# Optimization experiments

Hardware: AMD Instinct MI355X
Metric: run time of the kernel (lower is better)

The kernel has to match this reference:

```python
import jax, jax.numpy as jnp
import numpy as np

BN_EPS = 1e-5


def setup_inputs() -> dict:
    key = jax.random.key(0)
    ks = jax.random.split(key, 6)
    N, E, D_IN, D_OUT = 100000, 625000, 128, 128
    x = jax.random.normal(ks[0], (N, D_IN), dtype=jnp.float32)
    edge_index = jax.random.randint(ks[1], (2, E), 0, N, dtype=jnp.int64)
    # Glorot-style init for GCNConv weight, uniform for linear (values only matter for correctness testing)
    W = jax.random.normal(ks[2], (D_IN, D_OUT), dtype=jnp.float32) * (1.0 / np.sqrt(D_IN))
    b = jnp.zeros((D_OUT,), dtype=jnp.float32)
    res_W = jax.random.normal(ks[3], (D_IN, D_OUT), dtype=jnp.float32) * (1.0 / np.sqrt(D_IN))
    res_b = jnp.zeros((D_OUT,), dtype=jnp.float32)
    bn_gamma = jnp.ones((D_OUT,), dtype=jnp.float32)
    bn_beta = jnp.zeros((D_OUT,), dtype=jnp.float32)
    return {"x": x, "edge_index": edge_index, "W": W, "b": b,
            "res_W": res_W, "res_b": res_b, "bn_gamma": bn_gamma, "bn_beta": bn_beta}


def _gcn_forward(x, edge_index, W, b, res_W, res_b, bn_gamma, bn_beta):
    N = x.shape[0]
    # ---- GCNConv: add self-loops, symmetric degree normalization (PyG defaults) ----
    loops = jnp.arange(N, dtype=edge_index.dtype)
    src = jnp.concatenate([edge_index[0], loops])  # row (source)
    dst = jnp.concatenate([edge_index[1], loops])  # col (target)
    ones = jnp.ones(src.shape[0], dtype=x.dtype)
    deg = jax.ops.segment_sum(ones, dst, num_segments=N)  # in-degree incl. self-loop
    deg_inv_sqrt = jnp.where(deg > 0, jax.lax.rsqrt(deg), 0.0)
    norm = deg_inv_sqrt[src] * deg_inv_sqrt[dst]  # [E+N]
    # transform first (dense GEMM), then gather/scale/scatter-add
    h = x @ W  # [N, D_OUT]
    msg = h[src] * norm[:, None]  # gather + scale
    agg = jax.ops.segment_sum(msg, dst, num_segments=N) + b  # scatter-add + bias
    # ---- residual: relu(linear(x)) ----
    res = jax.nn.relu(x @ res_W + res_b)
    y = agg + res
    # ---- dropout(p=0.0) is identity; BatchNorm1d (training mode, batch stats) ----
    mean = jnp.mean(y, axis=0)
    var = jnp.mean(jnp.square(y - mean), axis=0)  # biased variance, as in torch BN normalization
    y = (y - mean) * jax.lax.rsqrt(var + BN_EPS) * bn_gamma + bn_beta
    return y


def reference(x, edge_index, W, b, res_W, res_b, bn_gamma, bn_beta):
    return _gcn_forward(x, edge_index, W, b, res_W, res_b, bn_gamma, bn_beta)
```

## Files before the change

kernel.cpp:

```cpp
#include <hip/hip_runtime.h>
#include <math.h>

#define D 128
#define DW 64

typedef __attribute__((ext_vector_type(8))) short bf16x8;
typedef __attribute__((ext_vector_type(4))) float f32x4;
union U4 { uint4 u; bf16x8 f; };

__device__ __forceinline__ float blo(unsigned p){ return __uint_as_float(p << 16); }
__device__ __forceinline__ float bhi(unsigned p){ return __uint_as_float(p & 0xffff0000u); }
__device__ __forceinline__ unsigned bpack(float a, float b){
  unsigned x = __float_as_uint(a), y = __float_as_uint(b);
  x += 0x7fffu + ((x >> 16) & 1u);
  y += 0x7fffu + ((y >> 16) & 1u);
  return (x >> 16) | (y & 0xffff0000u);
}


__global__ void k_deg(const int* __restrict__ ei, int* __restrict__ cnt, int E){
  int e = blockIdx.x*256 + threadIdx.x;
  if (e < E) atomicAdd(cnt + ei[E + e], 1);
}

__global__ void k_scan1(const int* __restrict__ cnt, int* __restrict__ off,
                        int* __restrict__ bsum, int N){
  __shared__ int sm[256];
  int i = blockIdx.x*256 + threadIdx.x;
  int v = (i < N) ? cnt[i] : 0;
  int acc = v;
  sm[threadIdx.x] = acc;
  __syncthreads();
  for (int s = 1; s < 256; s <<= 1){
    int t = (threadIdx.x >= s) ? sm[threadIdx.x - s] : 0;
    __syncthreads();
    acc += t;
    sm[threadIdx.x] = acc;
    __syncthreads();
  }
  if (i < N) off[i] = acc - v;
  if (threadIdx.x == 255) bsum[blockIdx.x] = acc;
}

__global__ void k_scan2(int* __restrict__ bsum, int nb){
  __shared__ int sm[512];
  int v = (threadIdx.x < nb) ? bsum[threadIdx.x] : 0;
  int acc = v;
  sm[threadIdx.x] = acc;
  __syncthreads();
  for (int s = 1; s < 512; s <<= 1){
    int t = (threadIdx.x >= s) ? sm[threadIdx.x - s] : 0;
    __syncthreads();
    acc += t;
    sm[threadIdx.x] = acc;
    __syncthreads();
  }
  if (threadIdx.x < nb) bsum[threadIdx.x] = acc - v;
}

__global__ void k_scan3(int* __restrict__ off, const int* __restrict__ bsum,
                        int* __restrict__ cursor, int N){
  int i = blockIdx.x*256 + threadIdx.x;
  if (i < N){
    int o = off[i] + bsum[blockIdx.x];
    off[i] = o;
    cursor[i] = o;
  }
}

__global__ void k_prep(const float* __restrict__ x, const int* __restrict__ cnt,
                       unsigned* __restrict__ out_u, int N){
  int idx = blockIdx.x*256 + threadIdx.x;
  if (idx >= N*DW) return;
  int row = idx >> 6, col = idx & 63;
  float dis = rsqrtf((float)(cnt[row] + 1));
  float2 xv = reinterpret_cast<const float2*>(x)[idx];
  out_u[(size_t)row*128 + 64 + col] = bpack(xv.x * dis, xv.y * dis);
}

__global__ void k_wprep(const float* __restrict__ W, const float* __restrict__ RW,
                        unsigned* __restrict__ dst){
  int idx = blockIdx.x*256 + threadIdx.x;
  int m = idx >> 13;
  int w = idx & 8191;
  int c = w >> 6, kd = w & 63;
  const float* src = m ? RW : W;
  float a = src[(2*kd)*128 + c];
  float b = src[(2*kd+1)*128 + c];
  dst[(m<<13) + c*64 + (kd ^ ((c & 7) << 2))] = bpack(a, b);
}

__global__ void k_fill(const int* __restrict__ ei, int* __restrict__ cursor,
                       int* __restrict__ elist, int E){
  int e = blockIdx.x*256 + threadIdx.x;
  if (e < E){
    int d = ei[E + e];
    int pos = atomicAdd(cursor + d, 1);
    elist[pos] = ei[e];
  }
}

__global__ __launch_bounds__(256) void k_agg(unsigned* __restrict__ out_u,
    const int* __restrict__ elist, const int* __restrict__ off,
    const int* __restrict__ cnt, int N){
  const int lane = threadIdx.x & 63;
  int wid = blockIdx.x*4 + (threadIdx.x >> 6);
  const int nw = gridDim.x*4;
  for (int i = wid; i < N; i += nw){
    int node = __builtin_amdgcn_readfirstlane(i);
    int o = off[node];
    int c = cnt[node];
    float a0 = 0.f, a1 = 0.f;
    for (int j0 = 0; j0 < c; j0 += 64){
      int m = c - j0; if (m > 64) m = 64;
      int sid = (j0 + lane < c) ? elist[o + j0 + lane] : 0;
      for (int jj = 0; jj < m; ++jj){
        int s = __shfl(sid, jj);
        unsigned p = out_u[(size_t)s*128 + 64 + lane];
        a0 += blo(p); a1 += bhi(p);
      }
    }
    unsigned ps = out_u[(size_t)node*128 + 64 + lane];
    a0 += blo(ps); a1 += bhi(ps);
    float dis = rsqrtf((float)(c + 1));
    out_u[(size_t)node*128 + lane] = bpack(a0*dis, a1*dis);
  }
}

__global__ __launch_bounds__(512) void k_gemm(
    const unsigned* __restrict__ wsW,
    const float* __restrict__ bias, const float* __restrict__ rbias,
    const int* __restrict__ cnt,
    float* __restrict__ out, float* __restrict__ colsum, int N)
{
  __shared__ unsigned lds[16384];
  unsigned* out_u = reinterpret_cast<unsigned*>(out);
  for (int i = threadIdx.x; i < 16384; i += 512) lds[i] = wsW[i];
  __syncthreads();

  const int lane = threadIdx.x & 63;
  const int wave = threadIdx.x >> 6;
  const int lo = lane & 15, hi = lane >> 4;
  const int rowbase = (blockIdx.x * 8 + wave) * 16;

  float bcol[8], rbcol[8];
  #pragma unroll
  for (int ct = 0; ct < 8; ++ct){
    bcol[ct]  = bias[ct*16 + lo];
    rbcol[ct] = rbias[ct*16 + lo];
  }

  int arow = rowbase + lo; if (arow >= N) arow = N - 1;
  U4 aggF[4], xbF[4];
  #pragma unroll
  for (int kk = 0; kk < 4; ++kk){
    aggF[kk].u = *(const uint4*)&out_u[(size_t)arow*128 + kk*16 + hi*4];
    xbF[kk].u  = *(const uint4*)&out_u[(size_t)arow*128 + 64 + kk*16 + hi*4];
  }

  f32x4 accA[8], accR[8];
  #pragma unroll
  for (int ct = 0; ct < 8; ++ct){
    accA[ct] = (f32x4){0.f,0.f,0.f,0.f};
    accR[ct] = (f32x4){0.f,0.f,0.f,0.f};
  }

  #pragma unroll
  for (int ct = 0; ct < 8; ++ct){
    const int c = ct*16 + lo;
    #pragma unroll
    for (int kk = 0; kk < 4; ++kk){
      int kd = (kk*16 + hi*4) ^ ((c & 7) << 2);
      U4 wf, rf;
      wf.u = *(const uint4*)&lds[c*64 + kd];
      rf.u = *(const uint4*)&lds[8192 + c*64 + kd];
      accA[ct] = __builtin_amdgcn_mfma_f32_16x16x32_bf16(aggF[kk].f, wf.f, accA[ct], 0,0,0);
      accR[ct] = __builtin_amdgcn_mfma_f32_16x16x32_bf16(xbF[kk].f, rf.f, accR[ct], 0,0,0);
    }
  }

  float s_[4];
  #pragma unroll
  for (int j = 0; j < 4; ++j){
    int r = rowbase + hi*4 + j;
    int rc = r < N ? r : N - 1;
    s_[j] = sqrtf((float)(cnt[rc] + 1));
  }
  float cs[8], cq[8];
  #pragma unroll
  for (int ct = 0; ct < 8; ++ct){ cs[ct] = 0.f; cq[ct] = 0.f; }

  #pragma unroll
  for (int ct = 0; ct < 8; ++ct){
    const int col = ct*16 + lo;
    #pragma unroll
    for (int j = 0; j < 4; ++j){
      int r = rowbase + hi*4 + j;
      if (r < N){
        float y = accA[ct][j] + bcol[ct] + fmaxf(accR[ct][j]*s_[j] + rbcol[ct], 0.f);
        out[(size_t)r*128 + col] = y;
        cs[ct] += y; cq[ct] += y*y;
      }
    }
  }

  #pragma unroll
  for (int ct = 0; ct < 8; ++ct){
    cs[ct] += __shfl_xor(cs[ct], 16); cs[ct] += __shfl_xor(cs[ct], 32);
    cq[ct] += __shfl_xor(cq[ct], 16); cq[ct] += __shfl_xor(cq[ct], 32);
  }
  __syncthreads();
  float* red = reinterpret_cast<float*>(lds);
  if (lane < 16){
    #pragma unroll
    for (int ct = 0; ct < 8; ++ct){
      int col = ct*16 + lane;
      red[wave*256 + 2*col]     = cs[ct];
      red[wave*256 + 2*col + 1] = cq[ct];
    }
  }
  __syncthreads();
  if (threadIdx.x < 256){
    float t = 0.f;
    #pragma unroll
    for (int w = 0; w < 8; ++w) t += red[w*256 + threadIdx.x];
    atomicAdd(colsum + threadIdx.x, t);
  }
}

__global__ void k_bnfinal(const float* __restrict__ colsum, const float* __restrict__ gamma,
                          const float* __restrict__ beta, float* __restrict__ sc, float fN){
  int c = threadIdx.x;
  float mean = colsum[2*c] / fN;
  float var  = colsum[2*c + 1] / fN - mean*mean;
  var = fmaxf(var, 0.f);
  float inv = rsqrtf(var + 1e-5f);
  float s = gamma[c] * inv;
  sc[c] = s;
  sc[128 + c] = beta[c] - mean * s;
}

__global__ void k_norm(float4* __restrict__ out4, const float4* __restrict__ sc4, int n4){
  int idx = blockIdx.x*256 + threadIdx.x;
  int stride = gridDim.x*256;
  for (int i = idx; i < n4; i += stride){
    int cb = i & 31;
    float4 v = out4[i];
    float4 s = sc4[cb];
    float4 t = sc4[32 + cb];
    v.x = v.x*s.x + t.x; v.y = v.y*s.y + t.y;
    v.z = v.z*s.z + t.z; v.w = v.w*s.w + t.w;
    out4[i] = v;
  }
}

extern "C" void kernel_launch(void* const* d_in, const int* in_sizes, int n_in,
                              void* d_out, int out_size, void* d_ws, size_t ws_size,
                              hipStream_t stream){
  const float* x     = (const float*)d_in[0];
  const int*   ei    = (const int*)d_in[1];
  const float* W     = (const float*)d_in[2];
  const float* b     = (const float*)d_in[3];
  const float* RW    = (const float*)d_in[4];
  const float* rb    = (const float*)d_in[5];
  const float* gamma = (const float*)d_in[6];
  const float* beta  = (const float*)d_in[7];
  float* out = (float*)d_out;
  unsigned* out_u = (unsigned*)d_out;
  const int N = in_sizes[0] / D;
  const int E = in_sizes[1] / 2;

  char* ws = (char*)d_ws;
  size_t o = 0;
  auto alloc = [&](size_t bytes)->void*{
    void* p = ws + o;
    o += (bytes + 255) & ~size_t(255);
    return p;
  };
  int*      cnt    = (int*)alloc((size_t)N*4);
  int*      off    = (int*)alloc((size_t)N*4);
  int*      cursor = (int*)alloc((size_t)N*4);
  int*      bsum   = (int*)alloc(512*4);
  float*    colsum = (float*)alloc(256*4);
  float*    scale  = (float*)alloc(256*4);
  unsigned* wsW    = (unsigned*)alloc(16384*4);
  int*      elist  = (int*)alloc((size_t)E*4);

  hipMemsetAsync(cnt, 0, (size_t)N*4, stream);
  hipMemsetAsync(colsum, 0, 256*4, stream);

  int egrid = (E + 255)/256;
  int nb = (N + 255)/256;
  k_deg  <<<egrid, 256, 0, stream>>>(ei, cnt, E);
  k_scan1<<<nb,    256, 0, stream>>>(cnt, off, bsum, N);
  k_scan2<<<1,     512, 0, stream>>>(bsum, nb);
  k_scan3<<<nb,    256, 0, stream>>>(off, bsum, cursor, N);
  k_prep <<<(N*DW + 255)/256, 256, 0, stream>>>(x, cnt, out_u, N);
  k_wprep<<<64,    256, 0, stream>>>(W, RW, wsW);
  k_fill <<<egrid, 256, 0, stream>>>(ei, cursor, elist, E);
  k_agg  <<<4096,  256, 0, stream>>>(out_u, elist, off, cnt, N);
  k_gemm <<<(N + 127)/128, 512, 0, stream>>>(wsW, b, rb, cnt, out, colsum, N);
  k_bnfinal<<<1, 128, 0, stream>>>(colsum, gamma, beta, scale, (float)N);
  k_norm <<<2048, 256, 0, stream>>>((float4*)out, (const float4*)scale, N*32);
}
```

Measured before the change: 301.6 us.

## Unroll neighbor gathers, widen prep stores, fuse BN finalize into normalize

The aggregation loop now issues four independent neighbor-row loads per iteration instead of one, and hoists the self-row load, so more memory requests are in flight per wave. The prep kernel handles float4 inputs per thread and writes uint2 stores, halving its thread count. The separate BN-finalize launch is removed; every normalize block recomputes the per-column scale and shift into shared memory. The trade-offs are redundant scale computation in each of 2048 blocks and extra clamped or masked loads at tail iterations.

```diff
diff --git a/kernel.cpp b/kernel.cpp
--- a/kernel.cpp
+++ b/kernel.cpp
@@ -71,11 +71,12 @@
 __global__ void k_prep(const float* __restrict__ x, const int* __restrict__ cnt,
                        unsigned* __restrict__ out_u, int N){
   int idx = blockIdx.x*256 + threadIdx.x;
-  if (idx >= N*DW) return;
-  int row = idx >> 6, col = idx & 63;
+  if (idx >= N*32) return;
+  int row = idx >> 5, q = idx & 31;
   float dis = rsqrtf((float)(cnt[row] + 1));
-  float2 xv = reinterpret_cast<const float2*>(x)[idx];
-  out_u[(size_t)row*128 + 64 + col] = bpack(xv.x * dis, xv.y * dis);
+  float4 xv = reinterpret_cast<const float4*>(x)[idx];
+  uint2 r; r.x = bpack(xv.x*dis, xv.y*dis); r.y = bpack(xv.z*dis, xv.w*dis);
+  reinterpret_cast<uint2*>(out_u)[(size_t)row*64 + 32 + q] = r;
 }
 
 __global__ void k_wprep(const float* __restrict__ W, const float* __restrict__ RW,
@@ -110,17 +111,28 @@
     int node = __builtin_amdgcn_readfirstlane(i);
     int o = off[node];
     int c = cnt[node];
+    unsigned ps = out_u[(size_t)node*128 + 64 + lane];
     float a0 = 0.f, a1 = 0.f;
     for (int j0 = 0; j0 < c; j0 += 64){
       int m = c - j0; if (m > 64) m = 64;
-      int sid = (j0 + lane < c) ? elist[o + j0 + lane] : 0;
-      for (int jj = 0; jj < m; ++jj){
-        int s = __shfl(sid, jj);
-        unsigned p = out_u[(size_t)s*128 + 64 + lane];
-        a0 += blo(p); a1 += bhi(p);
+      int li = lane < m ? lane : m-1;
+      int sid = elist[o + j0 + li];
+      for (int jj = 0; jj < m; jj += 4){
+        int s0 = __shfl(sid, jj);
+        int s1 = __shfl(sid, jj+1 < m ? jj+1 : m-1);
+        int s2 = __shfl(sid, jj+2 < m ? jj+2 : m-1);
+        int s3 = __shfl(sid, jj+3 < m ? jj+3 : m-1);
+        unsigned p0 = out_u[(size_t)s0*128 + 64 + lane];
+        unsigned p1 = out_u[(size_t)s1*128 + 64 + lane];
+        unsigned p2 = out_u[(size_t)s2*128 + 64 + lane];
+        unsigned p3 = out_u[(size_t)s3*128 + 64 + lane];
+        if (jj+1 >= m) p1 = 0;
+        if (jj+2 >= m) p2 = 0;
+        if (jj+3 >= m) p3 = 0;
+        a0 += blo(p0) + blo(p1) + blo(p2) + blo(p3);
+        a1 += bhi(p0) + bhi(p1) + bhi(p2) + bhi(p3);
       }
     }
-    unsigned ps = out_u[(size_t)node*128 + 64 + lane];
     a0 += blo(ps); a1 += bhi(ps);
     float dis = rsqrtf((float)(c + 1));
     out_u[(size_t)node*128 + lane] = bpack(a0*dis, a1*dis);
@@ -228,26 +240,27 @@
   }
 }
 
-__global__ void k_bnfinal(const float* __restrict__ colsum, const float* __restrict__ gamma,
-                          const float* __restrict__ beta, float* __restrict__ sc, float fN){
-  int c = threadIdx.x;
-  float mean = colsum[2*c] / fN;
-  float var  = colsum[2*c + 1] / fN - mean*mean;
-  var = fmaxf(var, 0.f);
-  float inv = rsqrtf(var + 1e-5f);
-  float s = gamma[c] * inv;
-  sc[c] = s;
-  sc[128 + c] = beta[c] - mean * s;
-}
-
-__global__ void k_norm(float4* __restrict__ out4, const float4* __restrict__ sc4, int n4){
+__global__ void k_norm(float4* __restrict__ out4, const float* __restrict__ colsum,
+                       const float* __restrict__ gamma, const float* __restrict__ beta,
+                       float fN, int n4){
+  __shared__ float sc[256];
+  if (threadIdx.x < 128){
+    int c = threadIdx.x;
+    float mean = colsum[2*c] / fN;
+    float var  = fmaxf(colsum[2*c + 1] / fN - mean*mean, 0.f);
+    float s = gamma[c] * rsqrtf(var + 1e-5f);
+    sc[c] = s;
+    sc[128 + c] = beta[c] - mean * s;
+  }
+  __syncthreads();
+  const float4* s4 = reinterpret_cast<const float4*>(sc);
   int idx = blockIdx.x*256 + threadIdx.x;
   int stride = gridDim.x*256;
   for (int i = idx; i < n4; i += stride){
     int cb = i & 31;
     float4 v = out4[i];
-    float4 s = sc4[cb];
-    float4 t = sc4[32 + cb];
+    float4 s = s4[cb];
+    float4 t = s4[32 + cb];
     v.x = v.x*s.x + t.x; v.y = v.y*s.y + t.y;
     v.z = v.z*s.z + t.z; v.w = v.w*s.w + t.w;
     out4[i] = v;
@@ -282,7 +295,6 @@
   int*      cursor = (int*)alloc((size_t)N*4);
   int*      bsum   = (int*)alloc(512*4);
   float*    colsum = (float*)alloc(256*4);
-  float*    scale  = (float*)alloc(256*4);
   unsigned* wsW    = (unsigned*)alloc(16384*4);
   int*      elist  = (int*)alloc((size_t)E*4);
 
@@ -295,11 +307,10 @@
   k_scan1<<<nb,    256, 0, stream>>>(cnt, off, bsum, N);
   k_scan2<<<1,     512, 0, stream>>>(bsum, nb);
   k_scan3<<<nb,    256, 0, stream>>>(off, bsum, cursor, N);
-  k_prep <<<(N*DW + 255)/256, 256, 0, stream>>>(x, cnt, out_u, N);
+  k_prep <<<(N*32 + 255)/256, 256, 0, stream>>>(x, cnt, out_u, N);
   k_wprep<<<64,    256, 0, stream>>>(W, RW, wsW);
   k_fill <<<egrid, 256, 0, stream>>>(ei, cursor, elist, E);
   k_agg  <<<4096,  256, 0, stream>>>(out_u, elist, off, cnt, N);
   k_gemm <<<(N + 127)/128, 512, 0, stream>>>(wsW, b, rb, cnt, out, colsum, N);
-  k_bnfinal<<<1, 128, 0, stream>>>(colsum, gamma, beta, scale, (float)N);
-  k_norm <<<2048, 256, 0, stream>>>((float4*)out, (const float4*)scale, N*32);
-}
+  k_norm <<<2048,  256, 0, stream>>>((float4*)out, colsum, gamma, beta, (float)N, N*32);
+}
```

After: 269.9 us. -10.5%, faster.
